# Kernel tuning notes

Hardware: AMD Instinct MI355X
Metric: run time of the kernel (lower is better)

The kernel has to match this reference:

```python
import jax, jax.numpy as jnp
import numpy as np

B, S, D, H = 8, 1024, 1024, 16
DH = D // H  # 64

def setup_inputs() -> dict:
    key = jax.random.key(0)
    k1, k2, k3 = jax.random.split(key, 3)
    x = jax.random.normal(k1, (B, S, D), dtype=jnp.float32)
    mask = jnp.tril(jnp.ones((S, S), dtype=bool))[None, None]  # causal [1,1,S,S]
    W_qkv = jax.random.normal(k2, (D, 3 * D), dtype=jnp.float32) * 0.02
    W_out = jax.random.normal(k3, (D, D), dtype=jnp.float32) * 0.02
    return {"x": x, "mask": mask, "W_qkv": W_qkv, "W_out": W_out}

def reference(x, mask, W_qkv, W_out):
    qkv = jnp.einsum('bnd,de->bne', x, W_qkv)
    q, k, v = jnp.split(qkv, 3, axis=-1)
    # [b, h, n, dh]
    split_heads = lambda t: t.reshape(B, S, H, DH).transpose(0, 2, 1, 3)
    q, k, v = map(split_heads, (q, k, v))
    attn = jnp.einsum('bhnd,bhmd->bhnm', q, k) / jnp.sqrt(jnp.float32(DH))
    attn = jnp.where(mask, attn, 0.7 * jnp.finfo(attn.dtype).min)
    attn = jax.nn.softmax(attn.astype(jnp.float32), axis=-1).astype(x.dtype)
    out = jnp.einsum('bhnm,bhmd->bhnd', attn, v)
    out = out.transpose(0, 2, 1, 3).reshape(B, S, D)
    return jnp.einsum('bnd,de->bne', out, W_out)
```

## Files before the change

### kernel.cpp

```cpp
#include <hip/hip_runtime.h>
#include <stdint.h>

typedef __attribute__((ext_vector_type(8))) short short8;
typedef __attribute__((ext_vector_type(4))) float floatx4;

__device__ __forceinline__ unsigned short f2bf(float f) {
  union { float f; uint32_t u; } v; v.f = f;
  uint32_t u = v.u;
  return (unsigned short)((u + 0x7FFFu + ((u >> 16) & 1u)) >> 16);
}

__device__ __forceinline__ void gl_lds16(const void* g, void* l) {
  __builtin_amdgcn_global_load_lds((__attribute__((address_space(1))) void*)g,
                                   (__attribute__((address_space(3))) void*)l,
                                   16, 0, 0);
}

__global__ __launch_bounds__(256) void cast_x_kernel(const float* __restrict__ in,
                                                     unsigned short* __restrict__ out,
                                                     int n4) {
  int i = blockIdx.x * 256 + threadIdx.x;
  if (i >= n4) return;
  float4 v = ((const float4*)in)[i];
  ushort4 o;
  o.x = f2bf(v.x); o.y = f2bf(v.y); o.z = f2bf(v.z); o.w = f2bf(v.w);
  ((ushort4*)out)[i] = o;
}

__global__ __launch_bounds__(256) void transpose_cast_kernel(const float* __restrict__ in,
                                                             unsigned short* __restrict__ out,
                                                             int R, int C) {
  __shared__ float tile[32][33];
  int c0 = blockIdx.x * 32, r0 = blockIdx.y * 32;
  int tx = threadIdx.x & 31;
  int ty = threadIdx.x >> 5;
  for (int i = ty; i < 32; i += 8)
    tile[i][tx] = in[(size_t)(r0 + i) * C + c0 + tx];
  __syncthreads();
  for (int i = ty; i < 32; i += 8)
    out[(size_t)(c0 + i) * R + r0 + tx] = f2bf(tile[tx][i]);
}

__global__ __launch_bounds__(256) void gemm_bt_kernel(const unsigned short* __restrict__ A,
                                                      const unsigned short* __restrict__ Bt,
                                                      int N, int mode,
                                                      unsigned short* __restrict__ qo,
                                                      unsigned short* __restrict__ ko,
                                                      unsigned short* __restrict__ vo,
                                                      float* __restrict__ fo) {
  const int Kd = 1024;
  __shared__ unsigned short As[128 * 64];
  __shared__ unsigned short Bs[128 * 64];
  const int tid = threadIdx.x;
  const int w = tid >> 6, lane = tid & 63;
  const int quad = lane >> 4, l16 = lane & 15;
  const int l7 = l16 & 7;
  const int wm = w >> 1, wn = w & 1;
  const int m0 = blockIdx.y * 128, n0 = blockIdx.x * 128;
  const int tr = (mode == 0) && (n0 >= 2048);
  const int r8 = lane >> 3, ch = lane & 7;
  const int sw = (ch ^ r8) * 8;

  floatx4 acc[4][4];
#pragma unroll
  for (int i = 0; i < 4; ++i)
#pragma unroll
    for (int j = 0; j < 4; ++j)
      acc[i][j] = (floatx4){0.f, 0.f, 0.f, 0.f};

  for (int k0 = 0; k0 < Kd; k0 += 64) {
#pragma unroll
    for (int i = 0; i < 4; ++i) {
      const int row = i * 32 + w * 8 + r8;
      gl_lds16(A + (size_t)(m0 + row) * Kd + k0 + sw, (char*)As + i * 4096 + w * 1024);
      gl_lds16(Bt + (size_t)(n0 + row) * Kd + k0 + sw, (char*)Bs + i * 4096 + w * 1024);
    }
    __syncthreads();
#pragma unroll
    for (int half = 0; half < 2; ++half) {
      short8 af[4], bf[4];
#pragma unroll
      for (int i = 0; i < 4; ++i)
        af[i] = *(const short8*)((const char*)As + (wm * 64 + i * 16 + l16) * 128 +
                                 (((half << 2) | quad) ^ l7) * 16);
#pragma unroll
      for (int j = 0; j < 4; ++j)
        bf[j] = *(const short8*)((const char*)Bs + (wn * 64 + j * 16 + l16) * 128 +
                                 (((half << 2) | quad) ^ l7) * 16);
      if (!tr) {
#pragma unroll
        for (int i = 0; i < 4; ++i)
#pragma unroll
          for (int j = 0; j < 4; ++j)
            acc[i][j] = __builtin_amdgcn_mfma_f32_16x16x32_bf16(af[i], bf[j], acc[i][j], 0, 0, 0);
      } else {
#pragma unroll
        for (int p = 0; p < 4; ++p)
#pragma unroll
          for (int q = 0; q < 4; ++q)
            acc[p][q] = __builtin_amdgcn_mfma_f32_16x16x32_bf16(bf[p], af[q], acc[p][q], 0, 0, 0);
      }
    }
    __syncthreads();
  }

  if (tr) {
#pragma unroll
    for (int p = 0; p < 4; ++p)
#pragma unroll
      for (int q = 0; q < 4; ++q)
#pragma unroll
        for (int r = 0; r < 4; ++r) {
          int n = n0 + wn * 64 + p * 16 + quad * 4 + r;
          int m = m0 + wm * 64 + q * 16 + l16;
          int n1 = n & 1023;
          int h = n1 >> 6, dh = n1 & 63;
          int bb = m >> 10, s = m & 1023;
          vo[(size_t)(bb * 16 + h) * 65536 + (size_t)dh * 1024 + s] = f2bf(acc[p][q][r]);
        }
  } else {
#pragma unroll
    for (int i = 0; i < 4; ++i)
#pragma unroll
      for (int j = 0; j < 4; ++j)
#pragma unroll
        for (int r = 0; r < 4; ++r) {
          int m = m0 + wm * 64 + i * 16 + quad * 4 + r;
          int n = n0 + wn * 64 + j * 16 + l16;
          float v = acc[i][j][r];
          if (mode == 0) {
            int sec = n >> 10, n1 = n & 1023;
            int h = n1 >> 6, dh = n1 & 63;
            int bb = m >> 10, s = m & 1023;
            size_t base = (size_t)(bb * 16 + h) * 65536;
            unsigned short bv = f2bf(v);
            if (sec == 0) qo[base + (size_t)s * 64 + dh] = bv;
            else          ko[base + (size_t)s * 64 + dh] = bv;
          } else {
            fo[(size_t)m * N + n] = v;
          }
        }
  }
}

__global__ __launch_bounds__(256, 3) void attn_kernel(const unsigned short* __restrict__ Qb,
                                                      const unsigned short* __restrict__ Kb,
                                                      const unsigned short* __restrict__ VbT,
                                                      unsigned short* __restrict__ AOb) {
  __shared__ unsigned short Kt[2][4096];
  __shared__ unsigned short Vt[2][4096];
  const int tid = threadIdx.x;
  const int w = tid >> 6, lane = tid & 63;
  const int quad = lane >> 4, l16 = lane & 15;
  const int l7 = l16 & 7;
  const int by = blockIdx.y;
  const int bb = by >> 4, hh = by & 15;
  const int blk = (int)gridDim.x - 1 - (int)blockIdx.x;
  const int qbase = blk * 128 + w * 32;
  const unsigned short* Qp = Qb + (size_t)by * 65536;
  const unsigned short* Kp = Kb + (size_t)by * 65536;
  const unsigned short* Vp = VbT + (size_t)by * 65536;

  short8 bq[2][2];
#pragma unroll
  for (int qt = 0; qt < 2; ++qt)
#pragma unroll
    for (int kh = 0; kh < 2; ++kh)
      bq[qt][kh] = *(const short8*)(Qp + (size_t)(qbase + qt * 16 + l16) * 64 + kh * 32 + quad * 8);

  floatx4 o[2][4];
#pragma unroll
  for (int qt = 0; qt < 2; ++qt)
#pragma unroll
    for (int dt = 0; dt < 4; ++dt) o[qt][dt] = (floatx4){0.f, 0.f, 0.f, 0.f};
  floatx4 psum[2];
  psum[0] = (floatx4){0.f, 0.f, 0.f, 0.f};
  psum[1] = (floatx4){0.f, 0.f, 0.f, 0.f};

  const int ntm = 2 * blk + 2;
  const int r8 = lane >> 3, ch = lane & 7;
  const int sw8 = (ch ^ r8) * 8;

  auto stage = [&](int t, int buf) {
    const int n0 = t * 64;
#pragma unroll
    for (int i = 0; i < 2; ++i) {
      const int c = w * 2 + i;
      const int row = c * 8 + r8;
      gl_lds16(Kp + (size_t)(n0 + row) * 64 + sw8, (char*)&Kt[buf][0] + c * 1024);
      gl_lds16(Vp + (size_t)row * 1024 + n0 + sw8, (char*)&Vt[buf][0] + c * 1024);
    }
  };

  stage(0, 0);
  __syncthreads();

  for (int t = 0; t < ntm; ++t) {
    const int buf = t & 1;
    if (t + 1 < ntm) stage(t + 1, buf ^ 1);
    const int n0 = t * 64;
    if (n0 <= qbase + 31) {
      const char* kbase = (const char*)&Kt[buf][0];
      const char* vbase = (const char*)&Vt[buf][0];
      short8 ak[4][2];
#pragma unroll
      for (int kt = 0; kt < 4; ++kt)
#pragma unroll
        for (int kh = 0; kh < 2; ++kh)
          ak[kt][kh] = *(const short8*)(kbase + (kt * 16 + l16) * 128 +
                                        (((kh << 2) | quad) ^ l7) * 16);
      short8 pa[2][2];
#pragma unroll
      for (int kt = 0; kt < 4; ++kt) {
#pragma unroll
        for (int qt = 0; qt < 2; ++qt) {
          floatx4 s = (floatx4){0.f, 0.f, 0.f, 0.f};
          s = __builtin_amdgcn_mfma_f32_16x16x32_bf16(ak[kt][0], bq[qt][0], s, 0, 0, 0);
          s = __builtin_amdgcn_mfma_f32_16x16x32_bf16(ak[kt][1], bq[qt][1], s, 0, 0, 0);
          const int query = qbase + qt * 16 + l16;
#pragma unroll
          for (int r = 0; r < 4; ++r) {
            const int key = n0 + kt * 16 + quad * 4 + r;
            float e = __expf(fmaf(s[r], 0.125f, -8.0f));
            float p = (key <= query) ? e : 0.0f;
            psum[qt][r] += p;
            pa[qt][kt >> 1][(kt & 1) * 4 + r] = (short)f2bf(p);
          }
        }
      }
#pragma unroll
      for (int dt = 0; dt < 4; ++dt) {
        const int row128 = (dt * 16 + l16) * 128;
#pragma unroll
        for (int u = 0; u < 2; ++u) {
          union { short8 v8; ushort4 h[2]; } bv;
          bv.h[0] = *(const ushort4*)(vbase + row128 +
                                      (((u << 2) | (quad >> 1)) ^ l7) * 16 + (quad & 1) * 8);
          bv.h[1] = *(const ushort4*)(vbase + row128 +
                                      (((u << 2) | 2 | (quad >> 1)) ^ l7) * 16 + (quad & 1) * 8);
#pragma unroll
          for (int qt = 0; qt < 2; ++qt)
            o[qt][dt] = __builtin_amdgcn_mfma_f32_16x16x32_bf16(pa[qt][u], bv.v8, o[qt][dt], 0, 0, 0);
        }
      }
    }
    __syncthreads();
  }

#pragma unroll
  for (int qt = 0; qt < 2; ++qt) {
    float l = psum[qt][0] + psum[qt][1] + psum[qt][2] + psum[qt][3];
    l += __shfl_xor(l, 16);
    l += __shfl_xor(l, 32);
    float inv[4];
#pragma unroll
    for (int r = 0; r < 4; ++r)
      inv[r] = 1.0f / __shfl(l, quad * 4 + r);
#pragma unroll
    for (int dt = 0; dt < 4; ++dt)
#pragma unroll
      for (int r = 0; r < 4; ++r) {
        int row = qbase + qt * 16 + quad * 4 + r;
        AOb[(size_t)(bb * 1024 + row) * 1024 + hh * 64 + dt * 16 + l16] =
            f2bf(o[qt][dt][r] * inv[r]);
      }
  }
}

extern "C" void kernel_launch(void* const* d_in, const int* in_sizes, int n_in,
                              void* d_out, int out_size, void* d_ws, size_t ws_size,
                              hipStream_t stream) {
  const float* x    = (const float*)d_in[0];
  const float* Wqkv = (const float*)d_in[2];
  const float* Wout = (const float*)d_in[3];
  float* out = (float*)d_out;

  unsigned short* xb    = (unsigned short*)d_ws;
  unsigned short* WqkvT = xb    + (size_t)8 * 1024 * 1024;
  unsigned short* WoutT = WqkvT + (size_t)3 * 1024 * 1024;
  unsigned short* Qb    = WoutT + (size_t)1024 * 1024;
  unsigned short* Kb    = Qb    + (size_t)8 * 1024 * 1024;
  unsigned short* VbT   = Kb    + (size_t)8 * 1024 * 1024;
  unsigned short* AOb   = VbT   + (size_t)8 * 1024 * 1024;

  cast_x_kernel<<<8192, 256, 0, stream>>>(x, xb, 2097152);
  transpose_cast_kernel<<<dim3(96, 32), 256, 0, stream>>>(Wqkv, WqkvT, 1024, 3072);
  transpose_cast_kernel<<<dim3(32, 32), 256, 0, stream>>>(Wout, WoutT, 1024, 1024);
  gemm_bt_kernel<<<dim3(24, 64), 256, 0, stream>>>(xb, WqkvT, 3072, 0, Qb, Kb, VbT, nullptr);
  attn_kernel<<<dim3(8, 128), 256, 0, stream>>>(Qb, Kb, VbT, AOb);
  gemm_bt_kernel<<<dim3(8, 64), 256, 0, stream>>>(AOb, WoutT, 1024, 1, nullptr, nullptr, nullptr, out);
}
```

Baseline: 260.1 us.

## Double-buffer GEMM K-loop, stage epilogue through LDS, merge weight transposes

The GEMM kernel now double-buffers its A/B tiles in LDS, issuing the next K-slice's global-to-LDS loads before computing on the current one, which removes one barrier per iteration. Outputs go through an LDS staging tile so Q/K/V and the fp32 output are written with wide, coalesced vector stores instead of scattered 2-byte and 4-byte stores. The two weight transpose-cast launches are merged into one kernel, and the softmax exponent uses exp2f with pre-scaled constants. LDS use per GEMM block doubles to 64KB, which may reduce occupancy.

```diff
diff --git a/kernel.cpp b/kernel.cpp
--- a/kernel.cpp
+++ b/kernel.cpp
@@ -27,11 +27,17 @@
   ((ushort4*)out)[i] = o;
 }
 
-__global__ __launch_bounds__(256) void transpose_cast_kernel(const float* __restrict__ in,
-                                                             unsigned short* __restrict__ out,
-                                                             int R, int C) {
+__global__ __launch_bounds__(256) void transpose_cast2_kernel(const float* __restrict__ in0,
+                                                              unsigned short* __restrict__ out0,
+                                                              const float* __restrict__ in1,
+                                                              unsigned short* __restrict__ out1) {
   __shared__ float tile[32][33];
-  int c0 = blockIdx.x * 32, r0 = blockIdx.y * 32;
+  const int R = 1024;
+  int bx = blockIdx.x;
+  const float* in; unsigned short* out; int C;
+  if (bx < 96) { in = in0; out = out0; C = 3072; }
+  else         { in = in1; out = out1; C = 1024; bx -= 96; }
+  int c0 = bx * 32, r0 = blockIdx.y * 32;
   int tx = threadIdx.x & 31;
   int ty = threadIdx.x >> 5;
   for (int i = ty; i < 32; i += 8)
@@ -49,8 +55,11 @@
                                                       unsigned short* __restrict__ vo,
                                                       float* __restrict__ fo) {
   const int Kd = 1024;
-  __shared__ unsigned short As[128 * 64];
-  __shared__ unsigned short Bs[128 * 64];
+  __shared__ union {
+    struct { unsigned short A[2][8192]; unsigned short B[2][8192]; } s;
+    float cf[16384];
+    unsigned short ch[32768];
+  } sm;
   const int tid = threadIdx.x;
   const int w = tid >> 6, lane = tid & 63;
   const int quad = lane >> 4, l16 = lane & 15;
@@ -68,24 +77,34 @@
     for (int j = 0; j < 4; ++j)
       acc[i][j] = (floatx4){0.f, 0.f, 0.f, 0.f};
 
-  for (int k0 = 0; k0 < Kd; k0 += 64) {
+  auto stage = [&](int it, int buf) {
+    const int k0 = it * 64;
 #pragma unroll
     for (int i = 0; i < 4; ++i) {
       const int row = i * 32 + w * 8 + r8;
-      gl_lds16(A + (size_t)(m0 + row) * Kd + k0 + sw, (char*)As + i * 4096 + w * 1024);
-      gl_lds16(Bt + (size_t)(n0 + row) * Kd + k0 + sw, (char*)Bs + i * 4096 + w * 1024);
-    }
-    __syncthreads();
+      gl_lds16(A + (size_t)(m0 + row) * Kd + k0 + sw, (char*)&sm.s.A[buf][0] + i * 4096 + w * 1024);
+      gl_lds16(Bt + (size_t)(n0 + row) * Kd + k0 + sw, (char*)&sm.s.B[buf][0] + i * 4096 + w * 1024);
+    }
+  };
+
+  stage(0, 0);
+  __syncthreads();
+
+  for (int it = 0; it < 16; ++it) {
+    const int buf = it & 1;
+    if (it < 15) stage(it + 1, buf ^ 1);
+    const char* Ab = (const char*)&sm.s.A[buf][0];
+    const char* Bb = (const char*)&sm.s.B[buf][0];
 #pragma unroll
     for (int half = 0; half < 2; ++half) {
       short8 af[4], bf[4];
 #pragma unroll
       for (int i = 0; i < 4; ++i)
-        af[i] = *(const short8*)((const char*)As + (wm * 64 + i * 16 + l16) * 128 +
+        af[i] = *(const short8*)(Ab + (wm * 64 + i * 16 + l16) * 128 +
                                  (((half << 2) | quad) ^ l7) * 16);
 #pragma unroll
       for (int j = 0; j < 4; ++j)
-        bf[j] = *(const short8*)((const char*)Bs + (wn * 64 + j * 16 + l16) * 128 +
+        bf[j] = *(const short8*)(Bb + (wn * 64 + j * 16 + l16) * 128 +
                                  (((half << 2) | quad) ^ l7) * 16);
       if (!tr) {
 #pragma unroll
@@ -104,42 +123,63 @@
     __syncthreads();
   }
 
-  if (tr) {
-#pragma unroll
-    for (int p = 0; p < 4; ++p)
-#pragma unroll
-      for (int q = 0; q < 4; ++q)
-#pragma unroll
-        for (int r = 0; r < 4; ++r) {
-          int n = n0 + wn * 64 + p * 16 + quad * 4 + r;
-          int m = m0 + wm * 64 + q * 16 + l16;
-          int n1 = n & 1023;
-          int h = n1 >> 6, dh = n1 & 63;
-          int bb = m >> 10, s = m & 1023;
-          vo[(size_t)(bb * 16 + h) * 65536 + (size_t)dh * 1024 + s] = f2bf(acc[p][q][r]);
-        }
+  if (mode == 1) {
+    float* Cs = sm.cf;
+#pragma unroll
+    for (int i = 0; i < 4; ++i)
+#pragma unroll
+      for (int j = 0; j < 4; ++j)
+#pragma unroll
+        for (int r = 0; r < 4; ++r)
+          Cs[(wm * 64 + i * 16 + quad * 4 + r) * 128 + wn * 64 + j * 16 + l16] = acc[i][j][r];
+    __syncthreads();
+#pragma unroll
+    for (int c = 0; c < 16; ++c) {
+      int idx = c * 256 + tid;
+      float4 v = ((const float4*)sm.cf)[idx];
+      int row = idx >> 5, col = (idx & 31) * 4;
+      *(float4*)&fo[(size_t)(m0 + row) * N + n0 + col] = v;
+    }
   } else {
-#pragma unroll
-    for (int i = 0; i < 4; ++i)
-#pragma unroll
-      for (int j = 0; j < 4; ++j)
-#pragma unroll
-        for (int r = 0; r < 4; ++r) {
-          int m = m0 + wm * 64 + i * 16 + quad * 4 + r;
-          int n = n0 + wn * 64 + j * 16 + l16;
-          float v = acc[i][j][r];
-          if (mode == 0) {
-            int sec = n >> 10, n1 = n & 1023;
-            int h = n1 >> 6, dh = n1 & 63;
-            int bb = m >> 10, s = m & 1023;
-            size_t base = (size_t)(bb * 16 + h) * 65536;
-            unsigned short bv = f2bf(v);
-            if (sec == 0) qo[base + (size_t)s * 64 + dh] = bv;
-            else          ko[base + (size_t)s * 64 + dh] = bv;
-          } else {
-            fo[(size_t)m * N + n] = v;
-          }
-        }
+    unsigned short* Cs = sm.ch;
+    if (!tr) {
+#pragma unroll
+      for (int i = 0; i < 4; ++i)
+#pragma unroll
+        for (int j = 0; j < 4; ++j)
+#pragma unroll
+          for (int r = 0; r < 4; ++r)
+            Cs[(wm * 64 + i * 16 + quad * 4 + r) * 128 + wn * 64 + j * 16 + l16] =
+                f2bf(acc[i][j][r]);
+    } else {
+#pragma unroll
+      for (int p = 0; p < 4; ++p)
+#pragma unroll
+        for (int q = 0; q < 4; ++q)
+#pragma unroll
+          for (int r = 0; r < 4; ++r)
+            Cs[(wn * 64 + p * 16 + quad * 4 + r) * 128 + wm * 64 + q * 16 + l16] =
+                f2bf(acc[p][q][r]);
+    }
+    __syncthreads();
+    unsigned short* dst0 = (n0 < 1024) ? qo : ko;
+#pragma unroll
+    for (int c = 0; c < 8; ++c) {
+      int idx = c * 256 + tid;
+      short8 v = *(const short8*)((const char*)sm.ch + idx * 16);
+      int row = idx >> 4, col = (idx & 15) * 8;
+      if (!tr) {
+        int m = m0 + row, n = n0 + col;
+        int h = (n & 1023) >> 6, dh = n & 63;
+        int bb = m >> 10, s = m & 1023;
+        *(short8*)&dst0[(size_t)(bb * 16 + h) * 65536 + (size_t)s * 64 + dh] = v;
+      } else {
+        int n = n0 + row, m = m0 + col;
+        int h = (n & 1023) >> 6, dh = n & 63;
+        int bb = m >> 10, s0 = m & 1023;
+        *(short8*)&vo[(size_t)(bb * 16 + h) * 65536 + (size_t)dh * 1024 + s0] = v;
+      }
+    }
   }
 }
 
@@ -221,7 +261,7 @@
 #pragma unroll
           for (int r = 0; r < 4; ++r) {
             const int key = n0 + kt * 16 + quad * 4 + r;
-            float e = __expf(fmaf(s[r], 0.125f, -8.0f));
+            float e = exp2f(fmaf(s[r], 0.18033688f, -11.5415603f));
             float p = (key <= query) ? e : 0.0f;
             psum[qt][r] += p;
             pa[qt][kt >> 1][(kt & 1) * 4 + r] = (short)f2bf(p);
@@ -284,8 +324,7 @@
   unsigned short* AOb   = VbT   + (size_t)8 * 1024 * 1024;
 
   cast_x_kernel<<<8192, 256, 0, stream>>>(x, xb, 2097152);
-  transpose_cast_kernel<<<dim3(96, 32), 256, 0, stream>>>(Wqkv, WqkvT, 1024, 3072);
-  transpose_cast_kernel<<<dim3(32, 32), 256, 0, stream>>>(Wout, WoutT, 1024, 1024);
+  transpose_cast2_kernel<<<dim3(128, 32), 256, 0, stream>>>(Wqkv, WqkvT, Wout, WoutT);
   gemm_bt_kernel<<<dim3(24, 64), 256, 0, stream>>>(xb, WqkvT, 3072, 0, Qb, Kb, VbT, nullptr);
   attn_kernel<<<dim3(8, 128), 256, 0, stream>>>(Qb, Kb, VbT, AOb);
   gemm_bt_kernel<<<dim3(8, 64), 256, 0, stream>>>(AOb, WoutT, 1024, 1, nullptr, nullptr, nullptr, out);
```

After: 255.8 us. No clear change (-1.7%).
